# Kernel optimization log

Hardware: AMD Instinct MI355X
Metric: run time of the kernel (lower is better)

## Reference

```python
import jax, jax.numpy as jnp
import numpy as np

B, I, S, H, O = 128, 64, 2048, 128, 64


def setup_inputs() -> dict:
    key = jax.random.key(0)
    ks = jax.random.split(key, 9)
    sc = 0.1
    return {
        "x": jax.random.normal(ks[0], (B, I, S), dtype=jnp.float32),
        "Wx_out": jax.random.normal(ks[1], (I, 4 * H), dtype=jnp.float32) * sc,
        "Wh_out": jax.random.normal(ks[2], (H, 4 * H), dtype=jnp.float32) * sc,
        "b_out": jnp.zeros((4 * H,), dtype=jnp.float32),
        "Wx_in": jax.random.normal(ks[3], (H, 4 * H), dtype=jnp.float32) * sc,
        "Wh_in": jax.random.normal(ks[4], (H, 4 * H), dtype=jnp.float32) * sc,
        "b_in": jnp.zeros((4 * H,), dtype=jnp.float32),
        "W_lin": jax.random.normal(ks[5], (O, H), dtype=jnp.float32) * 0.01,
        "b_lin": jnp.zeros((O,), dtype=jnp.float32),
    }


def reference(x, Wx_out, Wh_out, b_out, Wx_in, Wh_in, b_in, W_lin, b_lin):
    # x: (B, I, S) -> permute(0,2,1) -> (B, S, I); scan over time axis.
    xs = jnp.transpose(x, (2, 0, 1))  # (S, B, I)
    h0 = jnp.zeros((x.shape[0], Wh_out.shape[0]), dtype=x.dtype)

    def step(carry, xt):
        h, c, cn = carry  # outer hidden, outer cell, inner cell
        gates = xt @ Wx_out + h @ Wh_out + b_out
        i, f, o, g = jnp.split(gates, 4, axis=-1)
        i, f, o = jax.nn.sigmoid(i), jax.nn.sigmoid(f), jax.nn.sigmoid(o)
        g = jnp.tanh(g)
        x_in = i * g          # inner LSTM input
        h_in = f * c          # inner LSTM hidden
        gi = x_in @ Wx_in + h_in @ Wh_in + b_in
        ii, fi, oi, gg = jnp.split(gi, 4, axis=-1)
        cn_new = jax.nn.sigmoid(fi) * cn + jax.nn.sigmoid(ii) * jnp.tanh(gg)
        c_new = jax.nn.sigmoid(oi) * jnp.tanh(cn_new)  # outer cell = inner hidden
        h_new = o * jnp.tanh(c_new)
        return (h_new, c_new, cn_new), h_new

    _, hs = jax.lax.scan(step, (h0, h0, h0), xs)  # hs: (S, B, H)
    hs = jnp.transpose(hs, (1, 0, 2))             # (B, S, H)
    return hs @ W_lin.T + b_lin                   # (B, S, O)
```

## Files before the change

### kernel.cpp

```cpp
#include <hip/hip_runtime.h>
#include <hip/hip_fp16.h>

#define BB 128
#define II 64
#define SS 2048
#define HH 128
#define GG 512
#define OO 64

typedef _Float16 f16x2 __attribute__((ext_vector_type(2)));
union F4H { float4 f4; f16x2 h[4]; };

__device__ __forceinline__ f16x2 pack2(float a, float b) {
    f16x2 r; r.x = (_Float16)a; r.y = (_Float16)b; return r;
}

__device__ __forceinline__ float dot2(f16x2 w, f16x2 v, float c) {
#if __has_builtin(__builtin_amdgcn_fdot2)
    return __builtin_amdgcn_fdot2(w, v, c, false);
#else
    return fmaf((float)w.x, (float)v.x, fmaf((float)w.y, (float)v.y, c));
#endif
}

__device__ __forceinline__ float tanh_f(float v) {
    float a = fabsf(v);
    float e = __expf(-2.0f * a);
    float r = (1.0f - e) * __builtin_amdgcn_rcpf(1.0f + e);
    return v < 0.0f ? -r : r;
}

template<int C>
__device__ __forceinline__ float qb(float v) {
    return __int_as_float(__builtin_amdgcn_mov_dpp(
        __float_as_int(v), 0x55 * C, 0xF, 0xF, true));
}
template<int N>
__device__ __forceinline__ float rolN(float v) {
    return __int_as_float(__builtin_amdgcn_mov_dpp(
        __float_as_int(v), 0x120 + (16 - N), 0xF, 0xF, true));
}

__device__ __forceinline__ void barrier_lds() {
    asm volatile("s_waitcnt lgkmcnt(0)\n\ts_barrier" ::: "memory");
}

__global__ void __launch_bounds__(512)
__attribute__((amdgpu_waves_per_eu(2)))
nlstm_scan(
    const float* __restrict__ x,
    const float* __restrict__ Wx_out, const float* __restrict__ Wh_out,
    const float* __restrict__ b_out,
    const float* __restrict__ Wx_in, const float* __restrict__ Wh_in,
    const float* __restrict__ b_in,
    const float* __restrict__ W_lin, const float* __restrict__ b_lin,
    float* __restrict__ out)
{
    const int b = blockIdx.x;
    const int j = threadIdx.x;
    const int u = j >> 2;
    const int g = j & 3;
    const int jcol = g * HH + u;

    __shared__ __align__(16) float4 wxf[8 * 512];
    __shared__ __align__(16) f16x2 xt[2][16][36];
    __shared__ __align__(16) f16x2 hb[HH / 2];
    __shared__ __align__(16) f16x2 xib[HH / 2];
    __shared__ __align__(16) f16x2 hib[HH / 2];

    f16x2 who[HH / 2];
    f16x2 wxi[HH / 2];
    f16x2 whi[HH / 2];
#pragma unroll
    for (int m = 0; m < HH / 2; ++m)
        who[m] = pack2(Wh_out[(2 * m) * GG + jcol], Wh_out[(2 * m + 1) * GG + jcol]);
#pragma unroll
    for (int m = 0; m < HH / 2; ++m)
        wxi[m] = pack2(Wx_in[(2 * m) * GG + jcol], Wx_in[(2 * m + 1) * GG + jcol]);
#pragma unroll
    for (int m = 0; m < HH / 2; ++m)
        whi[m] = pack2(Wh_in[(2 * m) * GG + jcol], Wh_in[(2 * m + 1) * GG + jcol]);

    const float bo  = b_out[jcol];
    const float bi2 = b_in[jcol];
    const int   pn = j >> 3;
    const int   ps = j & 7;
    const float bl = b_lin[pn];

    F4H wl[2];
#pragma unroll
    for (int q = 0; q < 2; ++q) {
        const int c = 2 * ps + q;
#pragma unroll
        for (int r = 0; r < 4; ++r)
            wl[q].h[r] = pack2(W_lin[pn * HH + 8 * c + 2 * r],
                               W_lin[pn * HH + 8 * c + 2 * r + 1]);
    }

#pragma unroll
    for (int c = 0; c < 8; ++c) {
        F4H w4;
#pragma unroll
        for (int q = 0; q < 4; ++q)
            w4.h[q] = pack2(Wx_out[(8 * c + 2 * q) * GG + jcol],
                            Wx_out[(8 * c + 2 * q + 1) * GG + jcol]);
        wxf[c * 512 + j] = w4.f4;
    }

    const float* xrow = x + (size_t)b * II * SS;
    float* orow = out + (size_t)b * SS * OO;

    const int xm  = j >> 4;
    const int xtl = j & 15;
    const float* xg0 = xrow + (size_t)(2 * xm) * SS + xtl;
    const float* xg1 = xrow + (size_t)(2 * xm + 1) * SS + xtl;

    xt[0][xtl][xm] = pack2(xg0[0], xg1[0]);
    if (j < HH / 2) hb[j] = pack2(0.f, 0.f);
    __syncthreads();

    float c_reg = 0.f, cn_reg = 0.f;

    const float4* hb4 = (const float4*)hb;
    const float4* xi4 = (const float4*)xib;
    const float4* hi4 = (const float4*)hib;
    const bool isT = (g == 3);

    float pr0 = 0.f, pr1 = 0.f;

#pragma unroll 1
    for (int t = 0; t < SS; ++t) {
        const int stl = t & 15;
        const int tb  = (t >> 4) & 1;

        if (stl == 0) {
            const int Tn = (t + 16 < SS) ? t + 16 : t;
            pr0 = xg0[Tn];
            pr1 = xg1[Tn];
        }

        const float4* xc4 = (const float4*)&xt[tb][stl][0];
        float a0 = 0.f, a1 = 0.f, a2 = 0.f, a3 = 0.f;
#pragma unroll
        for (int c = 0; c < 8; ++c) {
            F4H xu; xu.f4 = xc4[c];
            F4H wu; wu.f4 = wxf[c * 512 + j];
            a0 = dot2(wu.h[0], xu.h[0], a0);
            a1 = dot2(wu.h[1], xu.h[1], a1);
            a2 = dot2(wu.h[2], xu.h[2], a2);
            a3 = dot2(wu.h[3], xu.h[3], a3);
        }
#pragma unroll
        for (int c = 0; c < 16; ++c) {
            F4H hu; hu.f4 = hb4[c];
            a0 = dot2(who[4 * c + 0], hu.h[0], a0);
            a1 = dot2(who[4 * c + 1], hu.h[1], a1);
            a2 = dot2(who[4 * c + 2], hu.h[2], a2);
            a3 = dot2(who[4 * c + 3], hu.h[3], a3);
        }
        float acc = ((a0 + a1) + (a2 + a3)) + bo;

        float ap = isT ? 2.f * acc : acc;
        float s  = __builtin_amdgcn_rcpf(1.f + __expf(-ap));
        float av = isT ? fmaf(2.f, s, -1.f) : s;

        float vi = qb<0>(av), vf = qb<1>(av), vo = qb<2>(av), vg = qb<3>(av);
        float x_in    = vi * vg;
        float h_in    = vf * c_reg;
        float o_outer = vo;

        float p0 = 0.f, p1 = 0.f;
        {
            F4H hu0; hu0.f4 = hb4[2 * ps];
            F4H hu1; hu1.f4 = hb4[2 * ps + 1];
            p0 = dot2(wl[0].h[0], hu0.h[0], p0);
            p1 = dot2(wl[0].h[1], hu0.h[1], p1);
            p0 = dot2(wl[0].h[2], hu0.h[2], p0);
            p1 = dot2(wl[0].h[3], hu0.h[3], p1);
            p0 = dot2(wl[1].h[0], hu1.h[0], p0);
            p1 = dot2(wl[1].h[1], hu1.h[1], p1);
            p0 = dot2(wl[1].h[2], hu1.h[2], p0);
            p1 = dot2(wl[1].h[3], hu1.h[3], p1);
        }
        float p = p0 + p1;
        p += rolN<4>(p);
        p += rolN<2>(p);
        p += rolN<1>(p);
        if (ps == 0 && t > 0) orow[(size_t)(t - 1) * OO + pn] = p + bl;

        float xin_n = rolN<4>(x_in);
        float hin_n = rolN<4>(h_in);
        if ((j & 7) == 0) {
            xib[u >> 1] = pack2(x_in, xin_n);
            hib[u >> 1] = pack2(h_in, hin_n);
        }
        barrier_lds();

        float b0 = 0.f, b1 = 0.f, b2 = 0.f, b3 = 0.f;
#pragma unroll
        for (int c = 0; c < 16; ++c) {
            F4H xu; xu.f4 = xi4[c];
            b0 = dot2(wxi[4 * c + 0], xu.h[0], b0);
            b1 = dot2(wxi[4 * c + 1], xu.h[1], b1);
            b2 = dot2(wxi[4 * c + 2], xu.h[2], b2);
            b3 = dot2(wxi[4 * c + 3], xu.h[3], b3);
        }
#pragma unroll
        for (int c = 0; c < 16; ++c) {
            F4H hu; hu.f4 = hi4[c];
            b0 = dot2(whi[4 * c + 0], hu.h[0], b0);
            b1 = dot2(whi[4 * c + 1], hu.h[1], b1);
            b2 = dot2(whi[4 * c + 2], hu.h[2], b2);
            b3 = dot2(whi[4 * c + 3], hu.h[3], b3);
        }
        float acc2 = ((b0 + b1) + (b2 + b3)) + bi2;

        float ap2 = isT ? 2.f * acc2 : acc2;
        float s2  = __builtin_amdgcn_rcpf(1.f + __expf(-ap2));
        float av2 = isT ? fmaf(2.f, s2, -1.f) : s2;

        float ii = qb<0>(av2), fi = qb<1>(av2), oi = qb<2>(av2), gg = qb<3>(av2);
        float cn_new = fmaf(fi, cn_reg, ii * gg);
        cn_reg = cn_new;
        float c_new = oi * tanh_f(cn_new);
        c_reg = c_new;
        float h_new = o_outer * tanh_f(c_new);

        float hn_n = rolN<4>(h_new);
        if ((j & 7) == 0) hb[u >> 1] = pack2(h_new, hn_n);
        if (stl == 0) xt[tb ^ 1][xtl][xm] = pack2(pr0, pr1);
        barrier_lds();
    }

    {
        float p0 = 0.f, p1 = 0.f;
        F4H hu0; hu0.f4 = hb4[2 * ps];
        F4H hu1; hu1.f4 = hb4[2 * ps + 1];
        p0 = dot2(wl[0].h[0], hu0.h[0], p0);
        p1 = dot2(wl[0].h[1], hu0.h[1], p1);
        p0 = dot2(wl[0].h[2], hu0.h[2], p0);
        p1 = dot2(wl[0].h[3], hu0.h[3], p1);
        p0 = dot2(wl[1].h[0], hu1.h[0], p0);
        p1 = dot2(wl[1].h[1], hu1.h[1], p1);
        p0 = dot2(wl[1].h[2], hu1.h[2], p0);
        p1 = dot2(wl[1].h[3], hu1.h[3], p1);
        float p = p0 + p1;
        p += rolN<4>(p);
        p += rolN<2>(p);
        p += rolN<1>(p);
        if (ps == 0) orow[(size_t)(SS - 1) * OO + pn] = p + bl;
    }
}

extern "C" void kernel_launch(void* const* d_in, const int* in_sizes, int n_in,
                              void* d_out, int out_size, void* d_ws, size_t ws_size,
                              hipStream_t stream) {
    (void)in_sizes; (void)n_in; (void)d_ws; (void)ws_size; (void)out_size;
    const float* x      = (const float*)d_in[0];
    const float* Wx_out = (const float*)d_in[1];
    const float* Wh_out = (const float*)d_in[2];
    const float* b_out  = (const float*)d_in[3];
    const float* Wx_in  = (const float*)d_in[4];
    const float* Wh_in  = (const float*)d_in[5];
    const float* b_in   = (const float*)d_in[6];
    const float* W_lin  = (const float*)d_in[7];
    const float* b_lin  = (const float*)d_in[8];
    float* out = (float*)d_out;

    nlstm_scan<<<dim3(BB), dim3(512), 0, stream>>>(
        x, Wx_out, Wh_out, b_out, Wx_in, Wh_in, b_in, W_lin, b_lin, out);
}
```

Baseline: 4.034 ms.

## Batch input projection over 16 timesteps into LDS and split inner accumulators

The outer-gate input projection (x_t @ Wx_out) moves out of the per-step path. It is now computed for 16 timesteps at once each time a new x tile is staged, and the results are stored in a new LDS buffer. Each Wx fragment is then read from LDS once per 16 steps instead of every step, and the per-step critical path only reads one precomputed value. The inner-gate dot products also now use separate accumulator chains for the x and h halves to expose more ILP. The costs are 32KB more LDS, a heavier step every 16 iterations, and extra register pressure next to the 192 VGPRs of resident weights, which could cause spills.

```diff
diff --git a/kernel.cpp b/kernel.cpp
--- a/kernel.cpp
+++ b/kernel.cpp
@@ -63,6 +63,7 @@
     const int jcol = g * HH + u;
 
     __shared__ __align__(16) float4 wxf[8 * 512];
+    __shared__ __align__(16) float  xwg[16][GG];
     __shared__ __align__(16) f16x2 xt[2][16][36];
     __shared__ __align__(16) f16x2 hb[HH / 2];
     __shared__ __align__(16) f16x2 xib[HH / 2];
@@ -137,19 +138,28 @@
             const int Tn = (t + 16 < SS) ? t + 16 : t;
             pr0 = xg0[Tn];
             pr1 = xg1[Tn];
-        }
-
-        const float4* xc4 = (const float4*)&xt[tb][stl][0];
-        float a0 = 0.f, a1 = 0.f, a2 = 0.f, a3 = 0.f;
-#pragma unroll
-        for (int c = 0; c < 8; ++c) {
-            F4H xu; xu.f4 = xc4[c];
-            F4H wu; wu.f4 = wxf[c * 512 + j];
-            a0 = dot2(wu.h[0], xu.h[0], a0);
-            a1 = dot2(wu.h[1], xu.h[1], a1);
-            a2 = dot2(wu.h[2], xu.h[2], a2);
-            a3 = dot2(wu.h[3], xu.h[3], a3);
-        }
+
+            float xa16[16];
+#pragma unroll
+            for (int tt = 0; tt < 16; ++tt) xa16[tt] = bo;
+#pragma unroll
+            for (int c = 0; c < 8; ++c) {
+                F4H wu; wu.f4 = wxf[c * 512 + j];
+#pragma unroll
+                for (int tt = 0; tt < 16; ++tt) {
+                    F4H xu; xu.f4 = ((const float4*)&xt[tb][tt][0])[c];
+                    xa16[tt] = dot2(wu.h[0], xu.h[0], xa16[tt]);
+                    xa16[tt] = dot2(wu.h[1], xu.h[1], xa16[tt]);
+                    xa16[tt] = dot2(wu.h[2], xu.h[2], xa16[tt]);
+                    xa16[tt] = dot2(wu.h[3], xu.h[3], xa16[tt]);
+                }
+            }
+#pragma unroll
+            for (int tt = 0; tt < 16; ++tt) xwg[tt][j] = xa16[tt];
+        }
+
+        float a0 = xwg[stl][j];
+        float a1 = 0.f, a2 = 0.f, a3 = 0.f;
 #pragma unroll
         for (int c = 0; c < 16; ++c) {
             F4H hu; hu.f4 = hb4[c];
@@ -158,7 +168,7 @@
             a2 = dot2(who[4 * c + 2], hu.h[2], a2);
             a3 = dot2(who[4 * c + 3], hu.h[3], a3);
         }
-        float acc = ((a0 + a1) + (a2 + a3)) + bo;
+        float acc = (a0 + a1) + (a2 + a3);
 
         float ap = isT ? 2.f * acc : acc;
         float s  = __builtin_amdgcn_rcpf(1.f + __expf(-ap));
@@ -196,24 +206,25 @@
         }
         barrier_lds();
 
-        float b0 = 0.f, b1 = 0.f, b2 = 0.f, b3 = 0.f;
+        float c0 = bi2, c1 = 0.f, c2 = 0.f, c3 = 0.f;
+        float d0 = 0.f, d1 = 0.f, d2 = 0.f, d3 = 0.f;
 #pragma unroll
         for (int c = 0; c < 16; ++c) {
             F4H xu; xu.f4 = xi4[c];
-            b0 = dot2(wxi[4 * c + 0], xu.h[0], b0);
-            b1 = dot2(wxi[4 * c + 1], xu.h[1], b1);
-            b2 = dot2(wxi[4 * c + 2], xu.h[2], b2);
-            b3 = dot2(wxi[4 * c + 3], xu.h[3], b3);
+            c0 = dot2(wxi[4 * c + 0], xu.h[0], c0);
+            c1 = dot2(wxi[4 * c + 1], xu.h[1], c1);
+            c2 = dot2(wxi[4 * c + 2], xu.h[2], c2);
+            c3 = dot2(wxi[4 * c + 3], xu.h[3], c3);
         }
 #pragma unroll
         for (int c = 0; c < 16; ++c) {
             F4H hu; hu.f4 = hi4[c];
-            b0 = dot2(whi[4 * c + 0], hu.h[0], b0);
-            b1 = dot2(whi[4 * c + 1], hu.h[1], b1);
-            b2 = dot2(whi[4 * c + 2], hu.h[2], b2);
-            b3 = dot2(whi[4 * c + 3], hu.h[3], b3);
-        }
-        float acc2 = ((b0 + b1) + (b2 + b3)) + bi2;
+            d0 = dot2(whi[4 * c + 0], hu.h[0], d0);
+            d1 = dot2(whi[4 * c + 1], hu.h[1], d1);
+            d2 = dot2(whi[4 * c + 2], hu.h[2], d2);
+            d3 = dot2(whi[4 * c + 3], hu.h[3], d3);
+        }
+        float acc2 = ((c0 + c1) + (c2 + c3)) + ((d0 + d1) + (d2 + d3));
 
         float ap2 = isT ? 2.f * acc2 : acc2;
         float s2  = __builtin_amdgcn_rcpf(1.f + __expf(-ap2));
```

Result: slower. 7.610 ms (+88.7%).
